# Optimization experiments

Measured on AMD Instinct MI355X. Metric: run time of the kernel, lower is better.

Reference implementation:

```python
import jax, jax.numpy as jnp
import numpy as np

D_MODEL, NHEAD, D_K = 512, 8, 64
MIN_RBF, MAX_RBF = 0.1, 0.9
MIN_SPREAD, MAX_SPREAD, BASE = 1.0, 6.0, 20.0
LN_EPS = 1e-5


def _layernorm(x, w, b):
    mu = jnp.mean(x, axis=-1, keepdims=True)
    var = jnp.var(x, axis=-1, keepdims=True)
    return (x - mu) * jax.lax.rsqrt(var + LN_EPS) * w + b


def setup_inputs() -> dict:
    key = jax.random.key(0)
    ks = jax.random.split(key, 10)
    B, N = 1, 2048
    inp = {
        "q": jax.random.normal(ks[0], (B, N, D_MODEL), jnp.float32),
        "k": jax.random.normal(ks[1], (B, N, D_MODEL), jnp.float32),
        "v": jax.random.normal(ks[2], (B, N, D_MODEL), jnp.float32),
        "coords": jax.random.normal(ks[3], (B, N, 3), jnp.float32) * 3.0,
        "key_padding_mask": jnp.zeros((B, N), bool),
        # learned params (torch.randn init for projections, LN defaults)
        "q_proj": jax.random.normal(ks[4], (NHEAD, D_MODEL, D_K), jnp.float32),
        "k_proj": jax.random.normal(ks[5], (NHEAD, D_MODEL, D_K), jnp.float32),
        "v_proj": jax.random.normal(ks[6], (NHEAD, D_MODEL, D_K), jnp.float32),
        "q_ln_w": jnp.ones((D_K,), jnp.float32), "q_ln_b": jnp.zeros((D_K,), jnp.float32),
        "k_ln_w": jnp.ones((D_K,), jnp.float32), "k_ln_b": jnp.zeros((D_K,), jnp.float32),
        "v_ln_w": jnp.ones((D_K,), jnp.float32), "v_ln_b": jnp.zeros((D_K,), jnp.float32),
        "out_w": jax.random.normal(ks[7], (D_MODEL, D_MODEL), jnp.float32) / np.sqrt(D_MODEL),
        "out_b": jnp.zeros((D_MODEL,), jnp.float32),
    }
    return inp


def reference(q, k, v, coords, key_padding_mask,
              q_proj, k_proj, v_proj,
              q_ln_w, q_ln_b, k_ln_w, k_ln_b, v_ln_w, v_ln_b,
              out_w, out_b):
    B, N, _ = q.shape
    # per-head projections: [B,H,N,dk]
    Q = _layernorm(jnp.einsum('bnd,hdk->bhnk', q, q_proj), q_ln_w, q_ln_b)
    K = _layernorm(jnp.einsum('bnd,hdk->bhnk', k, k_proj), k_ln_w, k_ln_b)
    V = _layernorm(jnp.einsum('bnd,hdk->bhnk', v, v_proj), v_ln_w, v_ln_b)

    # head-specific gaussian spreads (torch.logspace(0,1,H,base) semantics)
    spreads = MIN_SPREAD + (MAX_SPREAD - MIN_SPREAD) * (BASE ** jnp.linspace(0.0, 1.0, NHEAD) - 1.0) / (BASE - 1.0)

    # pairwise squared distances [B,N,N] -> per-head RBF [B,H,N,N]
    d2 = jnp.sum((coords[:, :, None, :] - coords[:, None, :, :]) ** 2, axis=-1)
    rbf = jnp.exp(-d2[:, None, :, :] / (2.0 * spreads[None, :, None, None] ** 2))
    rbf = jnp.clip(rbf, MIN_RBF, MAX_RBF)

    # RBF-modulated scaled dot-product attention
    scores = jnp.einsum('bhik,bhjk->bhij', Q, K) / np.sqrt(D_K) * rbf
    scores = jnp.where(key_padding_mask[:, None, None, :], -1e9, scores)
    P = jax.nn.softmax(scores, axis=-1)
    out = jnp.einsum('bhij,bhjk->bhik', P, V)  # [B,H,N,dk]

    # torch: out.permute(0,2,3,1).reshape(B,N,d_model)
    out = jnp.transpose(out, (0, 2, 3, 1)).reshape(B, N, D_MODEL)
    return out @ out_w.T + out_b
```

## Files before the change

kernel.cpp:

```cpp
#include <hip/hip_runtime.h>
#include <math.h>

#define N_TOK 2048
#define D_MODEL 512
#define NHEAD 8
#define DK 64
#define LOG2E 1.44269504f
#define QSCALE 0.18033688f

typedef __attribute__((ext_vector_type(8))) short short8;
typedef __attribute__((ext_vector_type(4))) short short4v;
typedef __attribute__((ext_vector_type(4))) float f32x4;

__device__ __forceinline__ short f2bf(float x) {
    unsigned u = __float_as_uint(x);
    u = (u + 0x7fffu + ((u >> 16) & 1u)) >> 16;
    return (short)u;
}

__device__ __forceinline__ float bf2f(short s) {
    return __uint_as_float(((unsigned)(unsigned short)s) << 16);
}

__device__ __forceinline__ unsigned cvt_pk_bf16(float lo, float hi) {
    unsigned r;
    asm("v_cvt_pk_bf16_f32 %0, %1, %2" : "=v"(r) : "v"(lo), "v"(hi));
    return r;
}

__device__ __forceinline__ float head_c(int h) {
    float tt = (float)h * (1.0f / 7.0f);
    float sp = 1.0f + 5.0f * (__builtin_exp2f(tt * 4.3219281f) - 1.0f) * (1.0f / 19.0f);
    return -LOG2E / (2.0f * sp * sp);
}

__global__ __launch_bounds__(256) void prep_all_kernel(
    const float* __restrict__ q, const float* __restrict__ k,
    const float* __restrict__ v, const float* __restrict__ coords,
    const unsigned char* __restrict__ mask,
    const float* __restrict__ qp, const float* __restrict__ kp,
    const float* __restrict__ vp, const float* __restrict__ ow,
    short* __restrict__ Xbf, short* __restrict__ Wt, short* __restrict__ Wo,
    float4* __restrict__ ck4, float* __restrict__ mpen,
    unsigned* __restrict__ tflag)
{
    __shared__ float tile[64][65];
    const int bid = blockIdx.x;
    const int t = threadIdx.x;

    if (bid < 1536) {
        int i = bid * 256 + t;
        int tt = i >> 17;
        int rem = i & 131071;
        const float4* src = (const float4*)(tt == 0 ? q : (tt == 1 ? k : v));
        float4 a = src[rem * 2], b = src[rem * 2 + 1];
        short8 o;
        o[0] = f2bf(a.x); o[1] = f2bf(a.y); o[2] = f2bf(a.z); o[3] = f2bf(a.w);
        o[4] = f2bf(b.x); o[5] = f2bf(b.y); o[6] = f2bf(b.z); o[7] = f2bf(b.w);
        *(short8*)(Xbf + (size_t)i * 8) = o;
    } else if (bid < 1792) {
        int i = bid - 1536;
        int z = i >> 6;
        int bx = i & 7, by = (i >> 3) & 7;
        if (z == 3) {
            int m0 = bx * 64, j0 = by * 64, hh = by;
            for (int ii = t; ii < 4096; ii += 256) {
                int r = ii >> 6, kk = ii & 63;
                Wo[(size_t)(m0 + r) * 512 + j0 + kk] =
                    f2bf(ow[(size_t)(m0 + r) * 512 + kk * 8 + hh]);
            }
            return;
        }
        const float* src = z == 0 ? qp : (z == 1 ? kp : vp);
        const int h = bx, d0 = by * 64;
        for (int ii = t; ii < 4096; ii += 256) {
            int r = ii >> 6, c = ii & 63;
            tile[r][c] = src[((size_t)h * 512 + d0 + r) * 64 + c];
        }
        __syncthreads();
        short* W = Wt + (size_t)z * 512 * 512;
        for (int ii = t; ii < 4096; ii += 256) {
            int cr = ii >> 6, dc_ = ii & 63;
            W[(size_t)(h * 64 + cr) * 512 + d0 + dc_] = f2bf(tile[dc_][cr]);
        }
    } else {
        int j = (bid - 1792) * 256 + t;
        float x = coords[j * 3 + 0], y = coords[j * 3 + 1], z = coords[j * 3 + 2];
        unsigned char mk = mask[j];
        mpen[j] = mk ? -1e9f : 0.f;
        unsigned long long b = __ballot(mk != 0);
        if ((t & 63) == 0) tflag[j >> 6] = (b != 0ull) ? 1u : 0u;
        float n2 = x * x + y * y + z * z;
        #pragma unroll
        for (int h = 0; h < NHEAD; ++h) {
            float c = head_c(h);
            float4 o; o.x = -2.f * c * x; o.y = -2.f * c * y; o.z = -2.f * c * z; o.w = c * n2;
            ck4[(size_t)h * N_TOK + j] = o;
        }
    }
}

__global__ __launch_bounds__(256) void proj_ln_mfma_kernel(
    const short* __restrict__ Xbf, const short* __restrict__ Wt,
    const float* __restrict__ qlw, const float* __restrict__ qlb,
    const float* __restrict__ klw, const float* __restrict__ klb,
    const float* __restrict__ vlw, const float* __restrict__ vlb,
    short* __restrict__ Qbf, short* __restrict__ Kf, short* __restrict__ Vf)
{
    __shared__ short Xs[64 * 64];
    __shared__ short Ws[64 * 64];
    const int z = blockIdx.z, h = blockIdx.y;
    const int n0 = blockIdx.x * 64;
    const int tid = threadIdx.x, w = tid >> 6, l = tid & 63;
    const int l15 = l & 15, lg = l >> 4;

    const short* X = Xbf + (size_t)z * N_TOK * D_MODEL;
    const short* Wz = Wt + ((size_t)z * 512 + h * 64) * 512;

    const f32x4 zero4 = {0.f, 0.f, 0.f, 0.f};
    f32x4 acc[4];
    #pragma unroll
    for (int dc = 0; dc < 4; ++dc) acc[dc] = zero4;

    for (int kb = 0; kb < 8; ++kb) {
        const int d0 = kb * 64;
        __syncthreads();
        #pragma unroll
        for (int i = 0; i < 2; ++i) {
            int c = tid + i * 256;
            int r = c >> 3, g = c & 7;
            short8 xv = *(const short8*)(X + (size_t)(n0 + r) * 512 + d0 + g * 8);
            *(short8*)(Xs + r * 64 + ((g * 8) ^ ((r & 7) << 3))) = xv;
            short8 wv = *(const short8*)(Wz + (size_t)r * 512 + d0 + g * 8);
            *(short8*)(Ws + r * 64 + ((g * 8) ^ ((r & 7) << 3))) = wv;
        }
        __syncthreads();
        const int arow = w * 16 + l15;
        short8 a0 = *(const short8*)(Xs + arow * 64 + ((lg * 8) ^ ((arow & 7) << 3)));
        short8 a1 = *(const short8*)(Xs + arow * 64 + ((32 + lg * 8) ^ ((arow & 7) << 3)));
        #pragma unroll
        for (int dc = 0; dc < 4; ++dc) {
            const int brow = dc * 16 + l15;
            short8 b0 = *(const short8*)(Ws + brow * 64 + ((lg * 8) ^ ((brow & 7) << 3)));
            acc[dc] = __builtin_amdgcn_mfma_f32_16x16x32_bf16(a0, b0, acc[dc], 0, 0, 0);
            short8 b1 = *(const short8*)(Ws + brow * 64 + ((32 + lg * 8) ^ ((brow & 7) << 3)));
            acc[dc] = __builtin_amdgcn_mfma_f32_16x16x32_bf16(a1, b1, acc[dc], 0, 0, 0);
        }
    }

    const float* lw  = z == 0 ? qlw : (z == 1 ? klw : vlw);
    const float* lbp = z == 0 ? qlb : (z == 1 ? klb : vlb);
    float wv_[4], bv_[4];
    #pragma unroll
    for (int dc = 0; dc < 4; ++dc) {
        wv_[dc] = lw[dc * 16 + l15];
        bv_[dc] = lbp[dc * 16 + l15];
    }
    float mu[4], rs[4];
    #pragma unroll
    for (int reg = 0; reg < 4; ++reg) {
        float s = acc[0][reg] + acc[1][reg] + acc[2][reg] + acc[3][reg];
        #pragma unroll
        for (int off = 1; off < 16; off <<= 1) s += __shfl_xor(s, off);
        float m = s * (1.0f / 64.0f);
        float ss = 0.f;
        #pragma unroll
        for (int dc = 0; dc < 4; ++dc) { float d = acc[dc][reg] - m; ss += d * d; }
        #pragma unroll
        for (int off = 1; off < 16; off <<= 1) ss += __shfl_xor(ss, off);
        mu[reg] = m;
        rs[reg] = rsqrtf(ss * (1.0f / 64.0f) + 1e-5f);
    }

    const int tile = n0 >> 6;
    if (z == 0) {
        #pragma unroll
        for (int dc = 0; dc < 4; ++dc)
            #pragma unroll
            for (int reg = 0; reg < 4; ++reg) {
                int n = n0 + w * 16 + lg * 4 + reg;
                float val = ((acc[dc][reg] - mu[reg]) * rs[reg] * wv_[dc] + bv_[dc]) * QSCALE;
                Qbf[((size_t)h * N_TOK + n) * DK + dc * 16 + l15] = f2bf(val);
            }
    } else if (z == 1) {
        short* Kh = Kf + (size_t)h * N_TOK * DK;
        #pragma unroll
        for (int dc = 0; dc < 4; ++dc) {
            int hf  = dc >> 1;
            int lgc = ((dc & 1) << 1) | (l15 >> 3);
            int e   = l15 & 7;
            size_t base = (size_t)tile * 4096 + (w * 2 + hf) * 512 + 16 * 8 * lgc + e;
            #pragma unroll
            for (int reg = 0; reg < 4; ++reg) {
                float val = (acc[dc][reg] - mu[reg]) * rs[reg] * wv_[dc] + bv_[dc];
                Kh[base + (lg * 4 + reg) * 8] = f2bf(val);
            }
        }
    } else {
        short* Vh = Vf + (size_t)h * N_TOK * DK;
        int hfv = w >> 1;
        int lgv = ((w & 1) << 1) | (lg >> 1);
        int eb  = (lg & 1) * 4;
        #pragma unroll
        for (int dc = 0; dc < 4; ++dc) {
            short4v p;
            #pragma unroll
            for (int reg = 0; reg < 4; ++reg)
                p[reg] = f2bf((acc[dc][reg] - mu[reg]) * rs[reg] * wv_[dc] + bv_[dc]);
            size_t addr = (size_t)tile * 4096 + (dc * 2 + hfv) * 512 + (l15 + 16 * lgv) * 8 + eb;
            *(short4v*)(Vh + addr) = p;
        }
    }
}

__global__ __launch_bounds__(256) void attn_kernel(
    const short* __restrict__ Qbf, const short* __restrict__ Kf,
    const short* __restrict__ Vf, const float* __restrict__ coords,
    const float4* __restrict__ ck4, const float* __restrict__ mpen,
    const unsigned* __restrict__ tflag,
    short* __restrict__ PO, float* __restrict__ PL)
{
    __shared__ short Pls[4][1024];
    __shared__ float bufO[2][64][17];
    __shared__ float bufL[2][64];

    const int tid = threadIdx.x;
    const int w = tid >> 6, l = tid & 63;
    const int l15 = l & 15, lg = l >> 4;
    const int bid = blockIdx.x;
    const int h  = bid & 7;
    const int nt = (bid >> 3) & 127;
    const int z  = bid >> 10;
    const int n0 = nt * 16;

    char* Pb = (char*)&Pls[w][0];
    const int psw = (l15 & 7) << 4;

    const short* Qrow = Qbf + ((size_t)h * N_TOK + n0 + l15) * DK + lg * 8;
    const short8 qf0 = *(const short8*)(Qrow);
    const short8 qf1 = *(const short8*)(Qrow + 32);

    const float ch = head_c(h);
    const float qx = coords[(n0 + l15) * 3 + 0];
    const float qy = coords[(n0 + l15) * 3 + 1];
    const float qz = coords[(n0 + l15) * 3 + 2];
    const float cq2 = ch * (qx * qx + qy * qy + qz * qz);
    const float4* ckh = ck4 + (size_t)h * N_TOK;

    short8 ones8;
    #pragma unroll
    for (int i = 0; i < 8; ++i) ones8[i] = (short)0x3F80;

    const f32x4 zero4 = {0.f, 0.f, 0.f, 0.f};
    f32x4 oacc[4];
    f32x4 oacc_l = zero4;
    #pragma unroll
    for (int i = 0; i < 4; ++i) oacc[i] = zero4;

    const short* Kfh = Kf + (size_t)h * N_TOK * DK;
    const short* Vfh = Vf + (size_t)h * N_TOK * DK;

    for (int t = 0; t < 4; ++t) {
        const int kt = (z * 4 + w) * 4 + t;
        const int kbase = kt * 64;
        const short* kp = Kfh + (size_t)kt * 4096 + l * 8;
        const short* vp = Vfh + (size_t)kt * 4096 + l * 8;

        f32x4 sacc[4];
        #pragma unroll
        for (int nc = 0; nc < 4; ++nc) {
            short8 k0 = *(const short8*)(kp + nc * 1024);
            short8 k1 = *(const short8*)(kp + nc * 1024 + 512);
            sacc[nc] = __builtin_amdgcn_mfma_f32_16x16x32_bf16(k0, qf0, zero4, 0, 0, 0);
            sacc[nc] = __builtin_amdgcn_mfma_f32_16x16x32_bf16(k1, qf1, sacc[nc], 0, 0, 0);
        }

        #pragma unroll
        for (int nc = 0; nc < 4; ++nc) {
            #pragma unroll
            for (int reg = 0; reg < 4; ++reg) {
                float4 c4 = ckh[kbase + nc * 16 + lg * 4 + reg];
                float arg = fmaf(c4.x, qx, fmaf(c4.y, qy, fmaf(c4.z, qz, c4.w))) + cq2;
                float rb = __builtin_exp2f(arg);
                rb = fminf(fmaxf(rb, 0.1f), 0.9f);
                sacc[nc][reg] *= rb;
            }
        }
        if (tflag[kt]) {
            #pragma unroll
            for (int nc = 0; nc < 4; ++nc)
                #pragma unroll
                for (int reg = 0; reg < 4; ++reg)
                    sacc[nc][reg] += mpen[kbase + nc * 16 + lg * 4 + reg];
        }

        #pragma unroll
        for (int nc = 0; nc < 4; ++nc) {
            float p0 = __builtin_exp2f(sacc[nc][0]);
            float p1 = __builtin_exp2f(sacc[nc][1]);
            float p2 = __builtin_exp2f(sacc[nc][2]);
            float p3 = __builtin_exp2f(sacc[nc][3]);
            uint2 u;
            u.x = cvt_pk_bf16(p0, p1);
            u.y = cvt_pk_bf16(p2, p3);
            *(uint2*)(Pb + ((l15 * 128 + nc * 32 + lg * 8) ^ psw)) = u;
        }

        short8 pf0 = *(const short8*)(Pb + ((l15 * 128 + lg * 16) ^ psw));
        short8 pf1 = *(const short8*)(Pb + ((l15 * 128 + 64 + lg * 16) ^ psw));
        #pragma unroll
        for (int dcc = 0; dcc < 4; ++dcc) {
            short8 v0 = *(const short8*)(vp + dcc * 1024);
            short8 v1 = *(const short8*)(vp + dcc * 1024 + 512);
            oacc[dcc] = __builtin_amdgcn_mfma_f32_16x16x32_bf16(v0, pf0, oacc[dcc], 0, 0, 0);
            oacc[dcc] = __builtin_amdgcn_mfma_f32_16x16x32_bf16(v1, pf1, oacc[dcc], 0, 0, 0);
        }
        oacc_l = __builtin_amdgcn_mfma_f32_16x16x32_bf16(ones8, pf0, oacc_l, 0, 0, 0);
        oacc_l = __builtin_amdgcn_mfma_f32_16x16x32_bf16(ones8, pf1, oacc_l, 0, 0, 0);
    }

    float l_ = oacc_l[0];

    if (w >= 2) {
        int slot = w - 2;
        bufL[slot][l] = l_;
        #pragma unroll
        for (int dc = 0; dc < 4; ++dc)
            #pragma unroll
            for (int reg = 0; reg < 4; ++reg)
                bufO[slot][l][dc * 4 + reg] = oacc[dc][reg];
    }
    __syncthreads();
    if (w < 2) {
        l_ += bufL[w][l];
        #pragma unroll
        for (int dc = 0; dc < 4; ++dc)
            #pragma unroll
            for (int reg = 0; reg < 4; ++reg)
                oacc[dc][reg] += bufO[w][l][dc * 4 + reg];
    }
    __syncthreads();
    if (w == 1) {
        bufL[0][l] = l_;
        #pragma unroll
        for (int dc = 0; dc < 4; ++dc)
            #pragma unroll
            for (int reg = 0; reg < 4; ++reg)
                bufO[0][l][dc * 4 + reg] = oacc[dc][reg];
    }
    __syncthreads();
    if (w == 0) {
        float lf = l_ + bufL[0][l];
        size_t p = ((size_t)z * NHEAD + h) * N_TOK + n0 + l15;
        if (lg == 0) PL[p] = lf;
        #pragma unroll
        for (int dcc = 0; dcc < 4; ++dcc) {
            short4v o4;
            #pragma unroll
            for (int reg = 0; reg < 4; ++reg)
                o4[reg] = f2bf(oacc[dcc][reg] + bufO[0][l][dcc * 4 + reg]);
            *(short4v*)(PO + p * 64 + dcc * 16 + lg * 4) = o4;
        }
    }
}

__global__ __launch_bounds__(256) void out_proj_kernel(
    const short* __restrict__ PO, const float* __restrict__ PL,
    const short* __restrict__ Wo, const float* __restrict__ bias,
    float* __restrict__ out)
{
    __shared__ short As[64 * 64];
    __shared__ short Bs[64 * 64];
    const int n0 = blockIdx.x * 64, m0 = blockIdx.y * 64;
    const int tid = threadIdx.x, w = tid >> 6, l = tid & 63;
    const int l15 = l & 15, lg = l >> 4;

    const f32x4 zero4 = {0.f, 0.f, 0.f, 0.f};
    f32x4 acc[4];
    #pragma unroll
    for (int dc = 0; dc < 4; ++dc) acc[dc] = zero4;

    for (int kb = 0; kb < 8; ++kb) {
        const int j0 = kb * 64;
        __syncthreads();
        #pragma unroll
        for (int i = 0; i < 2; ++i) {
            int c = tid + i * 256;
            int r = c >> 3, g = c & 7;
            int n = n0 + r;
            size_t p0 = (size_t)kb * N_TOK + n;
            size_t p1 = (size_t)(NHEAD + kb) * N_TOK + n;
            float rl = 1.0f / (PL[p0] + PL[p1]);
            short8 a0 = *(const short8*)(PO + p0 * 64 + g * 8);
            short8 a1 = *(const short8*)(PO + p1 * 64 + g * 8);
            short8 av;
            #pragma unroll
            for (int e = 0; e < 8; ++e)
                av[e] = f2bf((bf2f(a0[e]) + bf2f(a1[e])) * rl);
            *(short8*)(As + r * 64 + ((g * 8) ^ ((r & 7) << 3))) = av;
            short8 bv = *(const short8*)(Wo + (size_t)(m0 + r) * 512 + j0 + g * 8);
            *(short8*)(Bs + r * 64 + ((g * 8) ^ ((r & 7) << 3))) = bv;
        }
        __syncthreads();
        const int arow = w * 16 + l15;
        short8 a0 = *(const short8*)(As + arow * 64 + ((lg * 8) ^ ((arow & 7) << 3)));
        short8 a1 = *(const short8*)(As + arow * 64 + ((32 + lg * 8) ^ ((arow & 7) << 3)));
        #pragma unroll
        for (int dc = 0; dc < 4; ++dc) {
            const int brow = dc * 16 + l15;
            short8 b0 = *(const short8*)(Bs + brow * 64 + ((lg * 8) ^ ((brow & 7) << 3)));
            acc[dc] = __builtin_amdgcn_mfma_f32_16x16x32_bf16(a0, b0, acc[dc], 0, 0, 0);
            short8 b1 = *(const short8*)(Bs + brow * 64 + ((32 + lg * 8) ^ ((brow & 7) << 3)));
            acc[dc] = __builtin_amdgcn_mfma_f32_16x16x32_bf16(a1, b1, acc[dc], 0, 0, 0);
        }
    }

    #pragma unroll
    for (int dc = 0; dc < 4; ++dc) {
        float bm = bias[m0 + dc * 16 + l15];
        #pragma unroll
        for (int reg = 0; reg < 4; ++reg) {
            int n = n0 + w * 16 + lg * 4 + reg;
            out[(size_t)n * D_MODEL + m0 + dc * 16 + l15] = acc[dc][reg] + bm;
        }
    }
}

extern "C" void kernel_launch(void* const* d_in, const int* in_sizes, int n_in,
                              void* d_out, int out_size, void* d_ws, size_t ws_size,
                              hipStream_t stream)
{
    const float* q      = (const float*)d_in[0];
    const float* k      = (const float*)d_in[1];
    const float* v      = (const float*)d_in[2];
    const float* coords = (const float*)d_in[3];
    const unsigned char* mask = (const unsigned char*)d_in[4];
    const float* q_proj = (const float*)d_in[5];
    const float* k_proj = (const float*)d_in[6];
    const float* v_proj = (const float*)d_in[7];
    const float* q_ln_w = (const float*)d_in[8];
    const float* q_ln_b = (const float*)d_in[9];
    const float* k_ln_w = (const float*)d_in[10];
    const float* k_ln_b = (const float*)d_in[11];
    const float* v_ln_w = (const float*)d_in[12];
    const float* v_ln_b = (const float*)d_in[13];
    const float* out_w  = (const float*)d_in[14];
    const float* out_b  = (const float*)d_in[15];
    float* out = (float*)d_out;

    short* Xbf = (short*)d_ws;
    short* Wt  = Xbf + 3145728;
    short* Wo  = Wt + 786432;
    short* Qbf = Wo + 262144;
    short* Kf  = Qbf + 1048576;
    short* Vf  = Kf + 1048576;
    float*  fr   = (float*)(Vf + 1048576);
    float4* ck4  = (float4*)fr;
    float*  mpen = fr + 65536;
    unsigned* tflag = (unsigned*)(mpen + 2048);

    short* PO = Xbf;
    float* PL = (float*)Wt;

    prep_all_kernel<<<dim3(1800), dim3(256), 0, stream>>>(
        q, k, v, coords, mask, q_proj, k_proj, v_proj, out_w,
        Xbf, Wt, Wo, ck4, mpen, tflag);
    proj_ln_mfma_kernel<<<dim3(32, 8, 3), dim3(256), 0, stream>>>(
        Xbf, Wt, q_ln_w, q_ln_b, k_ln_w, k_ln_b, v_ln_w, v_ln_b, Qbf, Kf, Vf);
    attn_kernel<<<dim3(2048), dim3(256), 0, stream>>>(
        Qbf, Kf, Vf, coords, ck4, mpen, tflag, PO, PL);
    out_proj_kernel<<<dim3(32, 8), dim3(256), 0, stream>>>(PO, PL, Wo, out_b, out);
}
```

Baseline: 74.60 us.

## Compute RBF distance argument via augmented bf16 MFMA instead of scalar FMAs

The per-pair RBF exponent (a quadratic form in query and key coordinates) is now computed with one extra 16x16x32 bf16 MFMA per key chunk. Coordinates are split into hi/lo (and hi/mid/lo for the squared-norm term) bf16 parts and packed into an augmented K tile stored next to the K features, with a matching augmented Q fragment. This replaces the per-element float4 loads from ck4 and the scalar FMA chain. In exchange it grows the K buffer by half, adds one MFMA per chunk, and relies on the split-bf16 products staying accurate enough for the exp2.

```diff
diff --git a/kernel.cpp b/kernel.cpp
--- a/kernel.cpp
+++ b/kernel.cpp
@@ -7,6 +7,8 @@
 #define DK 64
 #define LOG2E 1.44269504f
 #define QSCALE 0.18033688f
+#define KTILE 6144
+#define KHEAD (32 * KTILE)
 
 typedef __attribute__((ext_vector_type(8))) short short8;
 typedef __attribute__((ext_vector_type(4))) short short4v;
@@ -20,6 +22,18 @@
 
 __device__ __forceinline__ float bf2f(short s) {
     return __uint_as_float(((unsigned)(unsigned short)s) << 16);
+}
+
+__device__ __forceinline__ void split2(float x, short& h_, short& l_) {
+    h_ = f2bf(x);
+    l_ = f2bf(x - bf2f(h_));
+}
+
+__device__ __forceinline__ void split3(float x, short& h_, short& m_, short& l_) {
+    h_ = f2bf(x);
+    float r = x - bf2f(h_);
+    m_ = f2bf(r);
+    l_ = f2bf(r - bf2f(m_));
 }
 
 __device__ __forceinline__ unsigned cvt_pk_bf16(float lo, float hi) {
@@ -41,7 +55,7 @@
     const float* __restrict__ qp, const float* __restrict__ kp,
     const float* __restrict__ vp, const float* __restrict__ ow,
     short* __restrict__ Xbf, short* __restrict__ Wt, short* __restrict__ Wo,
-    float4* __restrict__ ck4, float* __restrict__ mpen,
+    short* __restrict__ Kf, float* __restrict__ mpen,
     unsigned* __restrict__ tflag)
 {
     __shared__ float tile[64][65];
@@ -91,11 +105,33 @@
         unsigned long long b = __ballot(mk != 0);
         if ((t & 63) == 0) tflag[j >> 6] = (b != 0ull) ? 1u : 0u;
         float n2 = x * x + y * y + z * z;
+        const short one = (short)0x3F80;
+        const int kr = j & 15;
         #pragma unroll
         for (int h = 0; h < NHEAD; ++h) {
             float c = head_c(h);
-            float4 o; o.x = -2.f * c * x; o.y = -2.f * c * y; o.z = -2.f * c * z; o.w = c * n2;
-            ck4[(size_t)h * N_TOK + j] = o;
+            short ahx, alx, ahy, aly, ahz, alz, k2a, k2b, k2c;
+            split2(-2.f * c * x, ahx, alx);
+            split2(-2.f * c * y, ahy, aly);
+            split2(-2.f * c * z, ahz, alz);
+            split3(c * n2, k2a, k2b, k2c);
+            short8 g0, g1, g2;
+            g0[0] = ahx; g0[1] = alx; g0[2] = ahx; g0[3] = ahy;
+            g0[4] = aly; g0[5] = ahy; g0[6] = ahz; g0[7] = alz;
+            g1[0] = ahz; g1[1] = alx; g1[2] = aly; g1[3] = alz;
+            g1[4] = k2a; g1[5] = k2b; g1[6] = k2c; g1[7] = one;
+            g2[0] = one; g2[1] = one;
+            #pragma unroll
+            for (int e = 2; e < 8; ++e) g2[e] = 0;
+            short8 g3;
+            #pragma unroll
+            for (int e = 0; e < 8; ++e) g3[e] = 0;
+            short* base = Kf + (size_t)h * KHEAD + (size_t)(j >> 6) * KTILE
+                        + 4096 + (size_t)((j >> 4) & 3) * 512;
+            *(short8*)(base + (size_t)(0 * 16 + kr) * 8) = g0;
+            *(short8*)(base + (size_t)(1 * 16 + kr) * 8) = g1;
+            *(short8*)(base + (size_t)(2 * 16 + kr) * 8) = g2;
+            *(short8*)(base + (size_t)(3 * 16 + kr) * 8) = g3;
         }
     }
 }
@@ -183,13 +219,13 @@
                 Qbf[((size_t)h * N_TOK + n) * DK + dc * 16 + l15] = f2bf(val);
             }
     } else if (z == 1) {
-        short* Kh = Kf + (size_t)h * N_TOK * DK;
+        short* Kh = Kf + (size_t)h * KHEAD;
         #pragma unroll
         for (int dc = 0; dc < 4; ++dc) {
             int hf  = dc >> 1;
             int lgc = ((dc & 1) << 1) | (l15 >> 3);
             int e   = l15 & 7;
-            size_t base = (size_t)tile * 4096 + (w * 2 + hf) * 512 + 16 * 8 * lgc + e;
+            size_t base = (size_t)tile * KTILE + (w * 2 + hf) * 512 + 16 * 8 * lgc + e;
             #pragma unroll
             for (int reg = 0; reg < 4; ++reg) {
                 float val = (acc[dc][reg] - mu[reg]) * rs[reg] * wv_[dc] + bv_[dc];
@@ -216,8 +252,7 @@
 __global__ __launch_bounds__(256) void attn_kernel(
     const short* __restrict__ Qbf, const short* __restrict__ Kf,
     const short* __restrict__ Vf, const float* __restrict__ coords,
-    const float4* __restrict__ ck4, const float* __restrict__ mpen,
-    const unsigned* __restrict__ tflag,
+    const float* __restrict__ mpen, const unsigned* __restrict__ tflag,
     short* __restrict__ PO, float* __restrict__ PL)
 {
     __shared__ short Pls[4][1024];
@@ -245,7 +280,26 @@
     const float qy = coords[(n0 + l15) * 3 + 1];
     const float qz = coords[(n0 + l15) * 3 + 2];
     const float cq2 = ch * (qx * qx + qy * qy + qz * qz);
-    const float4* ckh = ck4 + (size_t)h * N_TOK;
+    short8 qaug;
+    {
+        const short one = (short)0x3F80;
+        short qhx, qlx, qhy, qly, qhz, qlz, q2a, q2b, q2c;
+        split2(qx, qhx, qlx);
+        split2(qy, qhy, qly);
+        split2(qz, qhz, qlz);
+        split3(cq2, q2a, q2b, q2c);
+        #pragma unroll
+        for (int e = 0; e < 8; ++e) qaug[e] = 0;
+        if (lg == 0) {
+            qaug[0] = qhx; qaug[1] = qhx; qaug[2] = qlx; qaug[3] = qhy;
+            qaug[4] = qhy; qaug[5] = qly; qaug[6] = qhz; qaug[7] = qhz;
+        } else if (lg == 1) {
+            qaug[0] = qlz; qaug[1] = qlx; qaug[2] = qly; qaug[3] = qlz;
+            qaug[4] = one; qaug[5] = one; qaug[6] = one; qaug[7] = q2a;
+        } else if (lg == 2) {
+            qaug[0] = q2b; qaug[1] = q2c;
+        }
+    }
 
     short8 ones8;
     #pragma unroll
@@ -257,31 +311,32 @@
     #pragma unroll
     for (int i = 0; i < 4; ++i) oacc[i] = zero4;
 
-    const short* Kfh = Kf + (size_t)h * N_TOK * DK;
+    const short* Kfh = Kf + (size_t)h * KHEAD;
     const short* Vfh = Vf + (size_t)h * N_TOK * DK;
 
     for (int t = 0; t < 4; ++t) {
         const int kt = (z * 4 + w) * 4 + t;
         const int kbase = kt * 64;
-        const short* kp = Kfh + (size_t)kt * 4096 + l * 8;
+        const short* kp = Kfh + (size_t)kt * KTILE + l * 8;
+        const short* ap = Kfh + (size_t)kt * KTILE + 4096 + l * 8;
         const short* vp = Vfh + (size_t)kt * 4096 + l * 8;
 
-        f32x4 sacc[4];
+        f32x4 sacc[4], aacc[4];
         #pragma unroll
         for (int nc = 0; nc < 4; ++nc) {
             short8 k0 = *(const short8*)(kp + nc * 1024);
             short8 k1 = *(const short8*)(kp + nc * 1024 + 512);
+            short8 ka = *(const short8*)(ap + nc * 512);
             sacc[nc] = __builtin_amdgcn_mfma_f32_16x16x32_bf16(k0, qf0, zero4, 0, 0, 0);
             sacc[nc] = __builtin_amdgcn_mfma_f32_16x16x32_bf16(k1, qf1, sacc[nc], 0, 0, 0);
+            aacc[nc] = __builtin_amdgcn_mfma_f32_16x16x32_bf16(ka, qaug, zero4, 0, 0, 0);
         }
 
         #pragma unroll
         for (int nc = 0; nc < 4; ++nc) {
             #pragma unroll
             for (int reg = 0; reg < 4; ++reg) {
-                float4 c4 = ckh[kbase + nc * 16 + lg * 4 + reg];
-                float arg = fmaf(c4.x, qx, fmaf(c4.y, qy, fmaf(c4.z, qz, c4.w))) + cq2;
-                float rb = __builtin_exp2f(arg);
+                float rb = __builtin_exp2f(aacc[nc][reg]);
                 rb = fminf(fmaxf(rb, 0.1f), 0.9f);
                 sacc[nc][reg] *= rb;
             }
@@ -453,10 +508,8 @@
     short* Wo  = Wt + 786432;
     short* Qbf = Wo + 262144;
     short* Kf  = Qbf + 1048576;
-    short* Vf  = Kf + 1048576;
-    float*  fr   = (float*)(Vf + 1048576);
-    float4* ck4  = (float4*)fr;
-    float*  mpen = fr + 65536;
+    short* Vf  = Kf + 1572864;
+    float* mpen = (float*)(Vf + 1048576);
     unsigned* tflag = (unsigned*)(mpen + 2048);
 
     short* PO = Xbf;
@@ -464,10 +517,10 @@
 
     prep_all_kernel<<<dim3(1800), dim3(256), 0, stream>>>(
         q, k, v, coords, mask, q_proj, k_proj, v_proj, out_w,
-        Xbf, Wt, Wo, ck4, mpen, tflag);
+        Xbf, Wt, Wo, Kf, mpen, tflag);
     proj_ln_mfma_kernel<<<dim3(32, 8, 3), dim3(256), 0, stream>>>(
         Xbf, Wt, q_ln_w, q_ln_b, k_ln_w, k_ln_b, v_ln_w, v_ln_b, Qbf, Kf, Vf);
     attn_kernel<<<dim3(2048), dim3(256), 0, stream>>>(
-        Qbf, Kf, Vf, coords, ck4, mpen, tflag, PO, PL);
+        Qbf, Kf, Vf, coords, mpen, tflag, PO, PL);
     out_proj_kernel<<<dim3(32, 8), dim3(256), 0, stream>>>(PO, PL, Wo, out_b, out);
 }
```

New measurement: 66.85 us. -10.4%, faster.
